# Kernel optimization log

Measured on AMD Instinct MI355X. Metric: run time of the kernel, lower is better.

Reference implementation:

```python
import jax, jax.numpy as jnp
import numpy as np

N = 50000   # nodes
E = 400000  # edges
DIN = 128   # input feature dim (layer_config[0])
D = 512     # hidden dim (hardcoded in Encoder)


def setup_inputs() -> dict:
    key = jax.random.key(0)
    ks = jax.random.split(key, 16)

    def lin(k, fan_in, fan_out):
        # Kaiming-uniform-ish init, stored as [in, out] so y = x @ W + b
        bound = 1.0 / np.sqrt(fan_in)
        return jax.random.uniform(k, (fan_in, fan_out), jnp.float32, -bound, bound)

    inp = {
        "x1": jax.random.normal(ks[0], (N, DIN), jnp.float32),
        "x2": jax.random.normal(ks[1], (N, DIN), jnp.float32),
        "edge_index_v1": jax.random.randint(ks[2], (2, E), 0, N, jnp.int64 if jax.config.jax_enable_x64 else jnp.int32),
        "edge_index_v2": jax.random.randint(ks[3], (2, E), 0, N, jnp.int64 if jax.config.jax_enable_x64 else jnp.int32),
        # SAGEConv layer 1 (DIN -> D): lin_l (on mean-aggregated neighbors, with bias), lin_r (on root, no bias)
        "l1_Wl": lin(ks[4], DIN, D), "l1_bl": jnp.zeros((D,), jnp.float32), "l1_Wr": lin(ks[5], DIN, D),
        # SAGEConv layer 2 (D -> D)
        "l2_Wl": lin(ks[6], D, D), "l2_bl": jnp.zeros((D,), jnp.float32), "l2_Wr": lin(ks[7], D, D),
        # SAGEConv layer 3 (D -> D)
        "l3_Wl": lin(ks[8], D, D), "l3_bl": jnp.zeros((D,), jnp.float32), "l3_Wr": lin(ks[9], D, D),
        # residual projections W, W2 (DIN -> D) with bias
        "W_w": lin(ks[10], DIN, D), "W_b": jnp.zeros((D,), jnp.float32),
        "W2_w": lin(ks[11], DIN, D), "W2_b": jnp.zeros((D,), jnp.float32),
        # shared PReLU slope (nn.PReLU default: 1 param, init 0.25)
        "prelu_a": jnp.float32(0.25),
    }
    return inp


def _sage(x, src, dst, Wl, bl, Wr):
    # PyG SAGEConv (mean aggr): out = lin_l(mean_{j in N(i)} x_j) + lin_r(x_i)
    n = x.shape[0]
    agg = jax.ops.segment_sum(x[src], dst, num_segments=n)          # [N, F] scatter-add of gathered messages
    cnt = jax.ops.segment_sum(jnp.ones((src.shape[0],), x.dtype), dst, num_segments=n)
    mean = agg / jnp.maximum(cnt, 1.0)[:, None]                      # isolated nodes -> 0
    return mean @ Wl + bl + x @ Wr


def _prelu(h, a):
    return jnp.where(h >= 0, h, a * h)


def _encode(x, ei, p):
    src, dst = ei[0], ei[1]
    a = p["prelu_a"]
    h1 = _prelu(_sage(x, src, dst, p["l1_Wl"], p["l1_bl"], p["l1_Wr"]), a)
    h2 = _prelu(_sage(h1 + x @ p["W_w"] + p["W_b"], src, dst, p["l2_Wl"], p["l2_bl"], p["l2_Wr"]), a)
    h3 = _prelu(_sage(h2 + h1 + x @ p["W2_w"] + p["W2_b"], src, dst, p["l3_Wl"], p["l3_bl"], p["l3_Wr"]), a)
    return h3


def reference(x1, x2, edge_index_v1, edge_index_v2,
              l1_Wl, l1_bl, l1_Wr, l2_Wl, l2_bl, l2_Wr, l3_Wl, l3_bl, l3_Wr,
              W_w, W_b, W2_w, W2_b, prelu_a):
    p = dict(l1_Wl=l1_Wl, l1_bl=l1_bl, l1_Wr=l1_Wr,
             l2_Wl=l2_Wl, l2_bl=l2_bl, l2_Wr=l2_Wr,
             l3_Wl=l3_Wl, l3_bl=l3_bl, l3_Wr=l3_Wr,
             W_w=W_w, W_b=W_b, W2_w=W2_w, W2_b=W2_b, prelu_a=prelu_a)
    z1 = _encode(x1, edge_index_v1, p)
    z2 = _encode(x2, edge_index_v2, p)
    return (z1, z2)
```

## Files before the change

kernel.cpp:

```cpp
#include <hip/hip_runtime.h>


#define NN 50000
#define N2 100000
#define NE 400000
#define E2 800000
#define DIN 128
#define DH 512
#define MPAD 100352

typedef __attribute__((ext_vector_type(4))) float f32x4;
typedef __attribute__((ext_vector_type(8))) short bf16x8;
typedef unsigned short u16;

__device__ __forceinline__ u16 f2bf(float f) {
    unsigned u = __float_as_uint(f);
    unsigned r = (u + 0x7fff + ((u >> 16) & 1)) >> 16;
    return (u16)r;
}
__device__ __forceinline__ float bf2f(u16 b) {
    return __uint_as_float((unsigned)b << 16);
}

__device__ __forceinline__ void gload16(const void* g, void* l) {
    __builtin_amdgcn_global_load_lds(
        (const __attribute__((address_space(1))) unsigned int*)g,
        (__attribute__((address_space(3))) unsigned int*)l, 16, 0, 0);
}


__global__ void k_zero_int(int* __restrict__ p, int n) {
    int i = blockIdx.x * 256 + threadIdx.x;
    if (i < n) p[i] = 0;
}

__global__ void k_deg(const int* __restrict__ dst, int* __restrict__ deg, int E, int off) {
    int e = blockIdx.x * 256 + threadIdx.x;
    if (e < E) atomicAdd(&deg[dst[e] + off], 1);
}

__global__ __launch_bounds__(1024) void k_scan1(
        const int* __restrict__ deg, int* __restrict__ rowptr,
        int* __restrict__ bsum, int n) {
    __shared__ int buf[1024];
    int i = blockIdx.x * 1024 + threadIdx.x;
    int v = (i < n) ? deg[i] : 0;
    buf[threadIdx.x] = v;
    __syncthreads();
    for (int off = 1; off < 1024; off <<= 1) {
        int t = (threadIdx.x >= off) ? buf[threadIdx.x - off] : 0;
        __syncthreads();
        buf[threadIdx.x] += t;
        __syncthreads();
    }
    if (i < n) rowptr[i] = buf[threadIdx.x] - v;
    if (threadIdx.x == 1023) bsum[blockIdx.x] = buf[1023];
}

__global__ __launch_bounds__(128) void k_scan2(int* __restrict__ bsum, int nb) {
    __shared__ int buf[128];
    int v = (threadIdx.x < nb) ? bsum[threadIdx.x] : 0;
    buf[threadIdx.x] = v;
    __syncthreads();
    for (int off = 1; off < 128; off <<= 1) {
        int t = (threadIdx.x >= off) ? buf[threadIdx.x - off] : 0;
        __syncthreads();
        buf[threadIdx.x] += t;
        __syncthreads();
    }
    if (threadIdx.x < nb) bsum[threadIdx.x] = buf[threadIdx.x] - v;
}

__global__ void k_scan3(int* __restrict__ rowptr, const int* __restrict__ bsum,
                        int* __restrict__ cursor, int n, int total) {
    int i = blockIdx.x * 256 + threadIdx.x;
    if (i < n) {
        int v = rowptr[i] + bsum[i >> 10];
        rowptr[i] = v;
        cursor[i] = v;
    }
    if (i == 0) rowptr[n] = total;
}

__global__ void k_fill(const int* __restrict__ src, const int* __restrict__ dst,
                       int* __restrict__ cursor, int* __restrict__ col, int E, int off) {
    int e = blockIdx.x * 256 + threadIdx.x;
    if (e < E) {
        int p = atomicAdd(&cursor[dst[e] + off], 1);
        col[p] = src[e] + off;
    }
}


__global__ void k_cast_bf(const float* __restrict__ x, u16* __restrict__ o, int n) {
    int i = (blockIdx.x * 256 + threadIdx.x) * 4;
    if (i + 3 < n) {
        float4 v = *(const float4*)&x[i];
        o[i + 0] = f2bf(v.x); o[i + 1] = f2bf(v.y);
        o[i + 2] = f2bf(v.z); o[i + 3] = f2bf(v.w);
    } else {
        for (int j = i; j < n; ++j) o[j] = f2bf(x[j]);
    }
}


__global__ void k_wt(const float* __restrict__ W, u16* __restrict__ Wt, int K, int N) {
    __shared__ float t[32][33];
    int bn = blockIdx.x * 32;
    int bk = blockIdx.y * 32;
    int x = threadIdx.x;
    int y = threadIdx.y;
    for (int i = y; i < 32; i += 8) t[i][x] = W[(size_t)(bk + i) * N + bn + x];
    __syncthreads();
    for (int i = y; i < 32; i += 8)
        Wt[(size_t)(bn + i) * K + bk + x] = f2bf(t[x][i]);
}


template<int D>
__global__ __launch_bounds__(256) void k_agg_bf(
        const u16* __restrict__ x, const int* __restrict__ rowptr,
        const int* __restrict__ col, u16* __restrict__ mean, int n) {
    int node = blockIdx.x * 4 + (threadIdx.x >> 6);
    if (node >= n) return;
    int lane = threadIdx.x & 63;
    int s = rowptr[node], e = rowptr[node + 1];
    float inv = (e > s) ? 1.0f / (float)(e - s) : 0.0f;
    if (D == 512) {
        float acc[8] = {};
        const u16* xp = x + lane * 8;
        auto accum = [&](uint4 v) {
            unsigned w[4] = { v.x, v.y, v.z, v.w };
#pragma unroll
            for (int q = 0; q < 4; ++q) {
                acc[2 * q + 0] += bf2f((u16)(w[q] & 0xffff));
                acc[2 * q + 1] += bf2f((u16)(w[q] >> 16));
            }
        };
        int j = s;
        for (; j + 4 <= e; j += 4) {
            int r0 = col[j], r1 = col[j + 1], r2 = col[j + 2], r3 = col[j + 3];
            uint4 v0 = *(const uint4*)(xp + (size_t)r0 * D);
            uint4 v1 = *(const uint4*)(xp + (size_t)r1 * D);
            uint4 v2 = *(const uint4*)(xp + (size_t)r2 * D);
            uint4 v3 = *(const uint4*)(xp + (size_t)r3 * D);
            accum(v0); accum(v1); accum(v2); accum(v3);
        }
        for (; j < e; ++j) {
            int r = col[j];
            accum(*(const uint4*)(xp + (size_t)r * D));
        }
        unsigned o[4];
#pragma unroll
        for (int q = 0; q < 4; ++q)
            o[q] = (unsigned)f2bf(acc[2 * q] * inv) |
                   ((unsigned)f2bf(acc[2 * q + 1] * inv) << 16);
        *(uint4*)(mean + (size_t)node * D + lane * 8) = make_uint4(o[0], o[1], o[2], o[3]);
    } else {
        float a0 = 0.f, a1 = 0.f;
        const u16* xp = x + lane * 2;
        int j = s;
        for (; j + 4 <= e; j += 4) {
            int r0 = col[j], r1 = col[j + 1], r2 = col[j + 2], r3 = col[j + 3];
            unsigned v0 = *(const unsigned*)(xp + (size_t)r0 * D);
            unsigned v1 = *(const unsigned*)(xp + (size_t)r1 * D);
            unsigned v2 = *(const unsigned*)(xp + (size_t)r2 * D);
            unsigned v3 = *(const unsigned*)(xp + (size_t)r3 * D);
            a0 += bf2f((u16)(v0 & 0xffff)) + bf2f((u16)(v1 & 0xffff))
                + bf2f((u16)(v2 & 0xffff)) + bf2f((u16)(v3 & 0xffff));
            a1 += bf2f((u16)(v0 >> 16)) + bf2f((u16)(v1 >> 16))
                + bf2f((u16)(v2 >> 16)) + bf2f((u16)(v3 >> 16));
        }
        for (; j < e; ++j) {
            unsigned v = *(const unsigned*)(xp + (size_t)col[j] * D);
            a0 += bf2f((u16)(v & 0xffff));
            a1 += bf2f((u16)(v >> 16));
        }
        unsigned o = (unsigned)f2bf(a0 * inv) | ((unsigned)f2bf(a1 * inv) << 16);
        *(unsigned*)(mean + (size_t)node * D + lane * 2) = o;
    }
}

#define MFMA_BF16(a, b, c) __builtin_amdgcn_mfma_f32_16x16x32_bf16(a, b, c, 0, 0, 0)


__global__ __launch_bounds__(256) void k_l1f(
        const u16* __restrict__ X, const u16* __restrict__ Mn,
        const u16* __restrict__ Wr1, const u16* __restrict__ Wl1,
        const u16* __restrict__ Ww,  const u16* __restrict__ Ww2,
        const float* __restrict__ bl1, const float* __restrict__ Wb,
        const float* __restrict__ W2b, const float* __restrict__ prelu_a,
        u16* xin2, u16* xp3, int M) {
    __shared__ __align__(16) char SH[65536];

    int tid = threadIdx.x;
    int wid = tid >> 6, lane = tid & 63;
    int wm = wid >> 1, wn = wid & 1;
    const int lm = lane & 15;
    const int kq = lane >> 4;

    int nwg = gridDim.x;
    int q = nwg >> 3;
    int swz = (blockIdx.x & 7) * q + (blockIdx.x >> 3);
    int m0 = (swz >> 3) * 128;
    int n0 = (swz & 7) * 64;

    f32x4 acch[4][2], accw[4][2], accw2[4][2];
#pragma unroll
    for (int mi = 0; mi < 4; ++mi)
#pragma unroll
        for (int ni = 0; ni < 2; ++ni) {
            acch[mi][ni] = (f32x4){0.f, 0.f, 0.f, 0.f};
            accw[mi][ni] = (f32x4){0.f, 0.f, 0.f, 0.f};
            accw2[mi][ni] = (f32x4){0.f, 0.f, 0.f, 0.f};
        }

    const u16* Bmat[4] = { Wr1, Wl1, Ww, Ww2 };

    auto stage = [&](int buf, int s) {
        int k0 = s * 32;
        char* base = SH + buf * 32768;
#pragma unroll
        for (int i = 0; i < 2; ++i) {
            int f = tid + i * 256;
            int row = f >> 2, g = f & 3;
            int gs = g ^ (row & 3);
            gload16(X + (size_t)(m0 + row) * DIN + k0 + gs * 8,
                    base + i * 4096 + wid * 1024);
        }
#pragma unroll
        for (int i = 0; i < 2; ++i) {
            int f = tid + i * 256;
            int row = f >> 2, g = f & 3;
            int gs = g ^ (row & 3);
            gload16(Mn + (size_t)(m0 + row) * DIN + k0 + gs * 8,
                    base + 8192 + i * 4096 + wid * 1024);
        }
#pragma unroll
        for (int m = 0; m < 4; ++m) {
            int row = tid >> 2, g = tid & 3;
            int gs = g ^ (row & 3);
            gload16(Bmat[m] + (size_t)(n0 + row) * DIN + k0 + gs * 8,
                    base + 16384 + m * 4096 + wid * 1024);
        }
    };

    stage(0, 0);
    __syncthreads();

    int cur = 0;
#pragma unroll 1
    for (int s = 0; s < 4; ++s) {
        if (s + 1 < 4) stage(cur ^ 1, s + 1);

        const char* base = SH + cur * 32768;
        bf16x8 ax[4], am[4];
#pragma unroll
        for (int mi = 0; mi < 4; ++mi) {
            int row = wm * 64 + mi * 16 + lm;
            int g = kq ^ (row & 3);
            ax[mi] = *(const bf16x8*)(base + row * 64 + g * 16);
            am[mi] = *(const bf16x8*)(base + 8192 + row * 64 + g * 16);
        }
#pragma unroll
        for (int m = 0; m < 4; ++m) {
            bf16x8 bfr[2];
#pragma unroll
            for (int ni = 0; ni < 2; ++ni) {
                int row = wn * 32 + ni * 16 + lm;
                int g = kq ^ (row & 3);
                bfr[ni] = *(const bf16x8*)(base + 16384 + m * 4096 + row * 64 + g * 16);
            }
#pragma unroll
            for (int mi = 0; mi < 4; ++mi)
#pragma unroll
                for (int ni = 0; ni < 2; ++ni) {
                    if (m == 0) acch[mi][ni]  = MFMA_BF16(ax[mi], bfr[ni], acch[mi][ni]);
                    if (m == 1) acch[mi][ni]  = MFMA_BF16(am[mi], bfr[ni], acch[mi][ni]);
                    if (m == 2) accw[mi][ni]  = MFMA_BF16(ax[mi], bfr[ni], accw[mi][ni]);
                    if (m == 3) accw2[mi][ni] = MFMA_BF16(ax[mi], bfr[ni], accw2[mi][ni]);
                }
        }
        __syncthreads();
        cur ^= 1;
    }

    float aslope = *prelu_a;
    float blv[2], wbv[2], w2bv[2];
#pragma unroll
    for (int ni = 0; ni < 2; ++ni) {
        int col = n0 + wn * 32 + ni * 16 + lm;
        blv[ni] = bl1[col]; wbv[ni] = Wb[col]; w2bv[ni] = W2b[col];
    }
    char* T = SH + wid * 4608;
#pragma unroll
    for (int pass = 0; pass < 2; ++pass) {
#pragma unroll
        for (int mi = 0; mi < 4; ++mi)
#pragma unroll
            for (int ni = 0; ni < 2; ++ni)
#pragma unroll
                for (int r2 = 0; r2 < 4; ++r2) {
                    float h = acch[mi][ni][r2] + blv[ni];
                    h = (h >= 0.f) ? h : aslope * h;
                    float v = (pass == 0) ? h + accw[mi][ni][r2] + wbv[ni]
                                          : h + accw2[mi][ni][r2] + w2bv[ni];
                    ((u16*)(T + (mi * 16 + kq * 4 + r2) * 72))[ni * 16 + lm] = f2bf(v);
                }
        u16* O = pass ? xp3 : xin2;
#pragma unroll
        for (int it = 0; it < 4; ++it) {
            int lrow = it * 16 + (lane >> 2), seg = lane & 3;
            uint4 d = *(const uint4*)(T + lrow * 72 + seg * 16);
            int grow = m0 + wm * 64 + lrow;
            if (grow < M)
                *(uint4*)(O + (size_t)grow * DH + n0 + wn * 32 + seg * 8) = d;
        }
    }
}


template<bool ADDEND, bool OUTF32>
__global__ __launch_bounds__(256, 4) void k_mfma(
        const u16* __restrict__ A1, const u16* __restrict__ B1t,
        const u16* __restrict__ A2, const u16* __restrict__ B2t,
        const float* __restrict__ bias, const u16* addend,
        const float* __restrict__ prelu_a,
        float* Cf, u16* Cb, int M) {
    constexpr int MI = 4;
    __shared__ __align__(16) char SH[36864];

    constexpr int NS = 32;

    int tid = threadIdx.x;
    int wid = tid >> 6, lane = tid & 63;
    int wm = wid >> 1, wn = wid & 1;
    const int lm = lane & 15;
    const int kq = lane >> 4;

    int nwg = gridDim.x;
    int q = nwg >> 3;
    int swz = (blockIdx.x & 7) * q + (blockIdx.x >> 3);
    int m0 = (swz >> 2) * 128;
    int n0 = (swz & 3) * 128;

    f32x4 acc[MI][4];
#pragma unroll
    for (int mi = 0; mi < MI; ++mi)
#pragma unroll
        for (int ni = 0; ni < 4; ++ni)
            acc[mi][ni] = (f32x4){0.f, 0.f, 0.f, 0.f};

    auto stage = [&](int buf, int s) {
        const u16* A; const u16* Bt; int k0;
        if (s < 16) { A = A1; Bt = B1t; k0 = s * 32; }
        else        { A = A2; Bt = B2t; k0 = (s - 16) * 32; }
#pragma unroll
        for (int i = 0; i < 2; ++i) {
            int f = tid + i * 256;
            int row = f >> 2, g = f & 3;
            gload16(A + (size_t)(m0 + row) * DH + k0 + g * 8,
                    SH + buf * 8192 + i * 4096 + wid * 1024);
        }
#pragma unroll
        for (int i = 0; i < 2; ++i) {
            int f = tid + i * 256;
            int row = f >> 2, g = f & 3;
            gload16(Bt + (size_t)(n0 + row) * DH + k0 + g * 8,
                    SH + 16384 + buf * 8192 + i * 4096 + wid * 1024);
        }
    };

    stage(0, 0);
    __syncthreads();

    int cur = 0;
#pragma unroll 1
    for (int s = 0; s < NS; ++s) {
        if (s + 1 < NS) stage(cur ^ 1, s + 1);

        const char* Ab = SH + cur * 8192;
        const char* Bb = SH + 16384 + cur * 8192;
        bf16x8 af[MI], bfr[4];
#pragma unroll
        for (int mi = 0; mi < MI; ++mi) {
            int row = wm * 64 + mi * 16 + lm;
            af[mi] = *(const bf16x8*)(Ab + row * 64 + kq * 16);
        }
#pragma unroll
        for (int ni = 0; ni < 4; ++ni) {
            int row = wn * 64 + ni * 16 + lm;
            bfr[ni] = *(const bf16x8*)(Bb + row * 64 + kq * 16);
        }
#pragma unroll
        for (int mi = 0; mi < MI; ++mi)
#pragma unroll
            for (int ni = 0; ni < 4; ++ni)
                acc[mi][ni] = MFMA_BF16(af[mi], bfr[ni], acc[mi][ni]);

        __syncthreads();
        cur ^= 1;
    }

    float aslope = *prelu_a;
    char* EPW = SH + wid * 9216;
    float bv[4];
#pragma unroll
    for (int ni = 0; ni < 4; ++ni)
        bv[ni] = bias[n0 + wn * 64 + ni * 16 + lm];

    if (!OUTF32) {
        u16* T = (u16*)EPW;
#pragma unroll
        for (int mq = 0; mq < 4; ++mq) {
#pragma unroll
            for (int ni = 0; ni < 4; ++ni)
#pragma unroll
                for (int r2 = 0; r2 < 4; ++r2) {
                    float v = acc[mq][ni][r2] + bv[ni];
                    v = (v >= 0.f) ? v : aslope * v;
                    T[(mq * 16 + kq * 4 + r2) * 72 + ni * 16 + lm] = f2bf(v);
                }
        }
#pragma unroll
        for (int it = 0; it < 8; ++it) {
            int lrow = it * 8 + (lane >> 3);
            int grow = m0 + wm * 64 + lrow;
            uint4 d = *(const uint4*)(T + lrow * 72 + (lane & 7) * 8);
            if (grow < M) {
                size_t off = (size_t)grow * DH + n0 + wn * 64 + (lane & 7) * 8;
                if (ADDEND) {
                    uint4 ad = *(const uint4*)(addend + off);
                    unsigned* dp = (unsigned*)&d;
                    const unsigned* ap = (const unsigned*)&ad;
#pragma unroll
                    for (int qq = 0; qq < 4; ++qq) {
                        float lo = bf2f((u16)(dp[qq] & 0xffff)) + bf2f((u16)(ap[qq] & 0xffff));
                        float hi = bf2f((u16)(dp[qq] >> 16)) + bf2f((u16)(ap[qq] >> 16));
                        dp[qq] = (unsigned)f2bf(lo) | ((unsigned)f2bf(hi) << 16);
                    }
                }
                *(uint4*)(Cb + off) = d;
            }
        }
    } else {
        float* T = (float*)EPW;
#pragma unroll
        for (int sp = 0; sp < 2; ++sp) {
#pragma unroll
            for (int mq = 0; mq < 2; ++mq) {
                int mi = sp * 2 + mq;
#pragma unroll
                for (int ni = 0; ni < 4; ++ni)
#pragma unroll
                    for (int r2 = 0; r2 < 4; ++r2) {
                        float v = acc[mi][ni][r2] + bv[ni];
                        v = (v >= 0.f) ? v : aslope * v;
                        T[(mq * 16 + kq * 4 + r2) * 68 + ni * 16 + lm] = v;
                    }
            }
#pragma unroll
            for (int it = 0; it < 8; ++it) {
                int lrow = it * 4 + (lane >> 4);
                int grow = m0 + wm * 64 + sp * 32 + lrow;
                float4 d = *(const float4*)(T + lrow * 68 + (lane & 15) * 4);
                if (grow < M)
                    *(float4*)(Cf + (size_t)grow * DH + n0 + wn * 64 + (lane & 15) * 4) = d;
            }
        }
    }
}


extern "C" void kernel_launch(void* const* d_in, const int* in_sizes, int n_in,
                              void* d_out, int out_size, void* d_ws, size_t ws_size,
                              hipStream_t stream) {
    const float* x1 = (const float*)d_in[0];
    const float* x2 = (const float*)d_in[1];
    const int* ei1 = (const int*)d_in[2];
    const int* ei2 = (const int*)d_in[3];
    const float* l1_Wl = (const float*)d_in[4];
    const float* l1_bl = (const float*)d_in[5];
    const float* l1_Wr = (const float*)d_in[6];
    const float* l2_Wl = (const float*)d_in[7];
    const float* l2_bl = (const float*)d_in[8];
    const float* l2_Wr = (const float*)d_in[9];
    const float* l3_Wl = (const float*)d_in[10];
    const float* l3_bl = (const float*)d_in[11];
    const float* l3_Wr = (const float*)d_in[12];
    const float* W_w = (const float*)d_in[13];
    const float* W_b = (const float*)d_in[14];
    const float* W2_w = (const float*)d_in[15];
    const float* W2_b = (const float*)d_in[16];
    const float* prelu_a = (const float*)d_in[17];

    u16* wb = (u16*)d_ws;
    u16* Wr1t = wb;
    u16* Wl1t = Wr1t + 512 * 128;
    u16* Wwt  = Wl1t + 512 * 128;
    u16* W2wt = Wwt  + 512 * 128;
    u16* Wl2t = W2wt + 512 * 128;
    u16* Wr2t = Wl2t + 512 * 512;
    u16* Wl3t = Wr2t + 512 * 512;
    u16* Wr3t = Wl3t + 512 * 512;
    u16* x_bf    = Wr3t + 512 * 512;
    u16* mean_bf = x_bf + (size_t)MPAD * DIN;
    u16* xin2_bf = mean_bf + (size_t)MPAD * DH;
    u16* xp3_bf  = xin2_bf + (size_t)MPAD * DH;
    int* iws    = (int*)(xp3_bf + (size_t)MPAD * DH);
    int* deg    = iws;
    int* rowptr = iws + N2;
    int* cursor = iws + 2 * N2 + 1;
    int* bsum   = iws + 3 * N2 + 1;
    int* colx   = iws + 3 * N2 + 129;

    float* out = (float*)d_out;

    dim3 wtb(32, 8);
    k_wt<<<dim3(16, 4),  wtb, 0, stream>>>(l1_Wr, Wr1t, DIN, DH);
    k_wt<<<dim3(16, 4),  wtb, 0, stream>>>(l1_Wl, Wl1t, DIN, DH);
    k_wt<<<dim3(16, 4),  wtb, 0, stream>>>(W_w,  Wwt,  DIN, DH);
    k_wt<<<dim3(16, 4),  wtb, 0, stream>>>(W2_w, W2wt, DIN, DH);
    k_wt<<<dim3(16, 16), wtb, 0, stream>>>(l2_Wl, Wl2t, DH, DH);
    k_wt<<<dim3(16, 16), wtb, 0, stream>>>(l2_Wr, Wr2t, DH, DH);
    k_wt<<<dim3(16, 16), wtb, 0, stream>>>(l3_Wl, Wl3t, DH, DH);
    k_wt<<<dim3(16, 16), wtb, 0, stream>>>(l3_Wr, Wr3t, DH, DH);

    const int NB = (N2 + 1023) / 1024;
    k_zero_int<<<(N2 + 255) / 256, 256, 0, stream>>>(deg, N2);
    k_deg<<<(NE + 255) / 256, 256, 0, stream>>>(ei1 + NE, deg, NE, 0);
    k_deg<<<(NE + 255) / 256, 256, 0, stream>>>(ei2 + NE, deg, NE, NN);
    k_scan1<<<NB, 1024, 0, stream>>>(deg, rowptr, bsum, N2);
    k_scan2<<<1, 128, 0, stream>>>(bsum, NB);
    k_scan3<<<(N2 + 255) / 256, 256, 0, stream>>>(rowptr, bsum, cursor, N2, E2);
    k_fill<<<(NE + 255) / 256, 256, 0, stream>>>(ei1, ei1 + NE, cursor, colx, NE, 0);
    k_fill<<<(NE + 255) / 256, 256, 0, stream>>>(ei2, ei2 + NE, cursor, colx, NE, NN);

    k_cast_bf<<<(NN * DIN / 4 + 255) / 256, 256, 0, stream>>>(x1, x_bf, NN * DIN);
    k_cast_bf<<<(NN * DIN / 4 + 255) / 256, 256, 0, stream>>>(x2, x_bf + (size_t)NN * DIN, NN * DIN);

    const int nwgL1 = (MPAD / 128) * 8;
    const int nwgB  = (MPAD / 128) * 4;
    const int aggGrid = (N2 + 3) / 4;

    k_agg_bf<DIN><<<aggGrid, 256, 0, stream>>>(x_bf, rowptr, colx, mean_bf, N2);
    k_l1f<<<nwgL1, 256, 0, stream>>>(x_bf, mean_bf, Wr1t, Wl1t, Wwt, W2wt,
                                     l1_bl, W_b, W2_b, prelu_a, xin2_bf, xp3_bf, N2);

    k_agg_bf<DH><<<aggGrid, 256, 0, stream>>>(xin2_bf, rowptr, colx, mean_bf, N2);
    k_mfma<true, false><<<nwgB, 256, 0, stream>>>(
        mean_bf, Wl2t, xin2_bf, Wr2t, l2_bl, xp3_bf, prelu_a, nullptr, xp3_bf, N2);

    k_agg_bf<DH><<<aggGrid, 256, 0, stream>>>(xp3_bf, rowptr, colx, mean_bf, N2);
    k_mfma<false, true><<<nwgB, 256, 0, stream>>>(
        mean_bf, Wl3t, xp3_bf, Wr3t, l3_bl, nullptr, prelu_a, out, nullptr, N2);
}
```

Before: 833.3 us.

## Reorder layer-3 SAGE to transform-then-aggregate with fused bias and PReLU epilogue

Layer 3 now computes P = h·Wl and Q = h·Wr in one MFMA GEMM that shares the A tile, then runs a single gather kernel that averages P over neighbors and adds Q, bias and PReLU, writing fp32 output. Because the mean is linear, applying Wl before aggregation is equivalent. This removes the separate mean buffer pass and its GEMM epilogue. In exchange the GEMM now produces two bf16 outputs, which adds write traffic and an extra bf16 rounding of P before the averaging. Since input and hidden width are both 512, the gather itself moves the same amount of data as before.

```diff
diff --git a/kernel.cpp b/kernel.cpp
--- a/kernel.cpp
+++ b/kernel.cpp
@@ -181,6 +181,61 @@
     }
 }
 
+
+__global__ __launch_bounds__(256) void k_agg_fin(
+        const u16* __restrict__ P, const u16* __restrict__ Q,
+        const int* __restrict__ rowptr, const int* __restrict__ col,
+        const float* __restrict__ bias, const float* __restrict__ prelu_a,
+        float* __restrict__ z, int n) {
+    int node = blockIdx.x * 4 + (threadIdx.x >> 6);
+    if (node >= n) return;
+    int lane = threadIdx.x & 63;
+    int s = rowptr[node], e = rowptr[node + 1];
+    float inv = (e > s) ? 1.0f / (float)(e - s) : 0.0f;
+
+    float acc[8] = {};
+    const u16* xp = P + lane * 8;
+    auto accum = [&](uint4 v) {
+        unsigned w[4] = { v.x, v.y, v.z, v.w };
+#pragma unroll
+        for (int q = 0; q < 4; ++q) {
+            acc[2 * q + 0] += bf2f((u16)(w[q] & 0xffff));
+            acc[2 * q + 1] += bf2f((u16)(w[q] >> 16));
+        }
+    };
+    int j = s;
+    for (; j + 4 <= e; j += 4) {
+        int r0 = col[j], r1 = col[j + 1], r2 = col[j + 2], r3 = col[j + 3];
+        uint4 v0 = *(const uint4*)(xp + (size_t)r0 * DH);
+        uint4 v1 = *(const uint4*)(xp + (size_t)r1 * DH);
+        uint4 v2 = *(const uint4*)(xp + (size_t)r2 * DH);
+        uint4 v3 = *(const uint4*)(xp + (size_t)r3 * DH);
+        accum(v0); accum(v1); accum(v2); accum(v3);
+    }
+    for (; j < e; ++j)
+        accum(*(const uint4*)(xp + (size_t)col[j] * DH));
+
+    uint4 qv = *(const uint4*)(Q + (size_t)node * DH + lane * 8);
+    unsigned qw[4] = { qv.x, qv.y, qv.z, qv.w };
+    float4 b0 = *(const float4*)&bias[lane * 8];
+    float4 b1 = *(const float4*)&bias[lane * 8 + 4];
+    float bb[8] = { b0.x, b0.y, b0.z, b0.w, b1.x, b1.y, b1.z, b1.w };
+    float aslope = *prelu_a;
+
+    float4 o0, o1;
+    float* oo[8] = { &o0.x, &o0.y, &o0.z, &o0.w, &o1.x, &o1.y, &o1.z, &o1.w };
+#pragma unroll
+    for (int c = 0; c < 8; ++c) {
+        float qf = (c & 1) ? bf2f((u16)(qw[c >> 1] >> 16))
+                           : bf2f((u16)(qw[c >> 1] & 0xffff));
+        float v = acc[c] * inv + qf + bb[c];
+        *oo[c] = (v >= 0.f) ? v : aslope * v;
+    }
+    float* zp = z + (size_t)node * DH + lane * 8;
+    *(float4*)zp = o0;
+    *(float4*)(zp + 4) = o1;
+}
+
 #define MFMA_BF16(a, b, c) __builtin_amdgcn_mfma_f32_16x16x32_bf16(a, b, c, 0, 0, 0)
 
 
@@ -468,6 +523,124 @@
                     *(float4*)(Cf + (size_t)grow * DH + n0 + wn * 64 + (lane & 15) * 4) = d;
             }
         }
+    }
+}
+
+
+__global__ __launch_bounds__(256, 3) void k_mfma3l(
+        const u16* __restrict__ A, const u16* __restrict__ Bl,
+        const u16* __restrict__ Br, u16* __restrict__ P, u16* __restrict__ Q,
+        int M) {
+    __shared__ __align__(16) char SH[49152];
+
+    constexpr int NS = 16;
+
+    int tid = threadIdx.x;
+    int wid = tid >> 6, lane = tid & 63;
+    int wm = wid >> 1, wn = wid & 1;
+    const int lm = lane & 15;
+    const int kq = lane >> 4;
+
+    int nwg = gridDim.x;
+    int q = nwg >> 3;
+    int swz = (blockIdx.x & 7) * q + (blockIdx.x >> 3);
+    int m0 = (swz >> 2) * 128;
+    int n0 = (swz & 3) * 128;
+
+    f32x4 accP[4][4], accQ[4][4];
+#pragma unroll
+    for (int mi = 0; mi < 4; ++mi)
+#pragma unroll
+        for (int ni = 0; ni < 4; ++ni) {
+            accP[mi][ni] = (f32x4){0.f, 0.f, 0.f, 0.f};
+            accQ[mi][ni] = (f32x4){0.f, 0.f, 0.f, 0.f};
+        }
+
+    auto stage = [&](int buf, int s) {
+        int k0 = s * 32;
+#pragma unroll
+        for (int i = 0; i < 2; ++i) {
+            int f = tid + i * 256;
+            int row = f >> 2, g = f & 3;
+            gload16(A + (size_t)(m0 + row) * DH + k0 + g * 8,
+                    SH + buf * 8192 + i * 4096 + wid * 1024);
+        }
+#pragma unroll
+        for (int i = 0; i < 2; ++i) {
+            int f = tid + i * 256;
+            int row = f >> 2, g = f & 3;
+            gload16(Bl + (size_t)(n0 + row) * DH + k0 + g * 8,
+                    SH + 16384 + buf * 8192 + i * 4096 + wid * 1024);
+        }
+#pragma unroll
+        for (int i = 0; i < 2; ++i) {
+            int f = tid + i * 256;
+            int row = f >> 2, g = f & 3;
+            gload16(Br + (size_t)(n0 + row) * DH + k0 + g * 8,
+                    SH + 32768 + buf * 8192 + i * 4096 + wid * 1024);
+        }
+    };
+
+    stage(0, 0);
+    __syncthreads();
+
+    int cur = 0;
+#pragma unroll 1
+    for (int s = 0; s < NS; ++s) {
+        if (s + 1 < NS) stage(cur ^ 1, s + 1);
+
+        const char* Ab  = SH + cur * 8192;
+        const char* Blb = SH + 16384 + cur * 8192;
+        const char* Brb = SH + 32768 + cur * 8192;
+        bf16x8 af[4], bl[4], br[4];
+#pragma unroll
+        for (int mi = 0; mi < 4; ++mi) {
+            int row = wm * 64 + mi * 16 + lm;
+            af[mi] = *(const bf16x8*)(Ab + row * 64 + kq * 16);
+        }
+#pragma unroll
+        for (int ni = 0; ni < 4; ++ni) {
+            int row = wn * 64 + ni * 16 + lm;
+            bl[ni] = *(const bf16x8*)(Blb + row * 64 + kq * 16);
+            br[ni] = *(const bf16x8*)(Brb + row * 64 + kq * 16);
+        }
+#pragma unroll
+        for (int mi = 0; mi < 4; ++mi)
+#pragma unroll
+            for (int ni = 0; ni < 4; ++ni) {
+                accP[mi][ni] = MFMA_BF16(af[mi], bl[ni], accP[mi][ni]);
+                accQ[mi][ni] = MFMA_BF16(af[mi], br[ni], accQ[mi][ni]);
+            }
+
+        __syncthreads();
+        cur ^= 1;
+    }
+
+    char* EPW = SH + wid * 9216;
+    u16* T = (u16*)EPW;
+#pragma unroll
+    for (int pass = 0; pass < 2; ++pass) {
+#pragma unroll
+        for (int mq = 0; mq < 4; ++mq) {
+#pragma unroll
+            for (int ni = 0; ni < 4; ++ni)
+#pragma unroll
+                for (int r2 = 0; r2 < 4; ++r2) {
+                    float v = (pass == 0) ? accP[mq][ni][r2] : accQ[mq][ni][r2];
+                    T[(mq * 16 + kq * 4 + r2) * 72 + ni * 16 + lm] = f2bf(v);
+                }
+        }
+        __syncthreads();
+        u16* O = pass ? Q : P;
+#pragma unroll
+        for (int it = 0; it < 8; ++it) {
+            int lrow = it * 8 + (lane >> 3);
+            int grow = m0 + wm * 64 + lrow;
+            uint4 d = *(const uint4*)(T + lrow * 72 + (lane & 7) * 8);
+            if (grow < M)
+                *(uint4*)(O + (size_t)grow * DH + n0 + wn * 64 + (lane & 7) * 8) = d;
+        }
+        __syncthreads();
     }
 }
 
@@ -551,7 +724,7 @@
     k_mfma<true, false><<<nwgB, 256, 0, stream>>>(
         mean_bf, Wl2t, xin2_bf, Wr2t, l2_bl, xp3_bf, prelu_a, nullptr, xp3_bf, N2);
 
-    k_agg_bf<DH><<<aggGrid, 256, 0, stream>>>(xp3_bf, rowptr, colx, mean_bf, N2);
-    k_mfma<false, true><<<nwgB, 256, 0, stream>>>(
-        mean_bf, Wl3t, xp3_bf, Wr3t, l3_bl, nullptr, prelu_a, out, nullptr, N2);
-}
+    k_mfma3l<<<nwgB, 256, 0, stream>>>(xp3_bf, Wl3t, Wr3t, mean_bf, xin2_bf, N2);
+    k_agg_fin<<<aggGrid, 256, 0, stream>>>(mean_bf, xin2_bf, rowptr, colx,
+                                           l3_bl, prelu_a, out, N2);
+}
```

Result: slower. 935.9 us (+12.3%).
